# Performance work log

Measured on AMD Instinct MI355X. Metric: run time of the kernel, lower is better.

Reference implementation:

```python
import jax, jax.numpy as jnp
import numpy as np

B, S, H, F, E, K = 4, 2048, 1024, 3584, 8, 2
CAP_FACTOR = 1.25


def setup_inputs() -> dict:
    key = jax.random.key(0)
    k1, k2, k3, k4, k5 = jax.random.split(key, 5)
    s_h = 1.0 / np.sqrt(H)
    s_f = 1.0 / np.sqrt(F)
    return {
        "hidden_states": jax.random.normal(k1, (B, S, H), dtype=jnp.float32),
        "gate_w": jax.random.normal(k2, (E, H), dtype=jnp.float32) * s_h,
        "w1": jax.random.normal(k3, (E, H, F), dtype=jnp.float32) * s_h,
        "w2": jax.random.normal(k4, (E, F, H), dtype=jnp.float32) * s_f,
        "w3": jax.random.normal(k5, (E, H, F), dtype=jnp.float32) * s_h,
    }


def _moe_forward(hidden_states, gate_w, w1, w2, w3):
    b, s, h = hidden_states.shape
    dtype = hidden_states.dtype
    x = hidden_states.reshape(-1, h)  # [B*S, H]
    router_logits = x @ gate_w.T  # [B*S, E]
    expert_weights = jax.nn.softmax(router_logits.astype(jnp.float32), axis=1)
    _, selected_experts = jax.lax.top_k(expert_weights, K)  # [B*S, K]

    top_k_idx = selected_experts.reshape(b, s, K)
    probs = expert_weights.reshape(b, s, E)

    capacity = int(s * K / E * CAP_FACTOR)  # expert capacity per batch

    # dispatch/combine masks (Mixtral 'dropping' implementation)
    expert_mask = jax.nn.one_hot(top_k_idx, E, dtype=jnp.int32)  # [b,s,K,E]
    mask_fused = expert_mask.reshape(b, s * K, E)
    count_fused = jnp.cumsum(mask_fused, axis=1)  # running count per expert
    count = count_fused.reshape(b, s, K, E)
    trunc_mask = expert_mask * (count <= capacity).astype(jnp.int32)
    combined_mask = trunc_mask.sum(axis=2)  # [b,s,E]
    masked_probs = probs * combined_mask  # drop over-capacity tokens

    pos_fused = mask_fused * count_fused
    pos = pos_fused.reshape(b, s, K, E)
    combined_pos = pos.sum(axis=2) * combined_mask  # [b,s,E], 1-based slot
    pos_in_cap = jax.nn.one_hot(combined_pos, capacity + 1, dtype=jnp.int32)
    combine_mask = masked_probs[..., None] * pos_in_cap  # [b,s,E,cap+1]
    combine_mask = combine_mask[..., 1:].astype(dtype)  # drop slot 0 (dropped tokens)
    dispatch_mask = (combine_mask != 0).astype(dtype)  # [b,s,E,cap]

    # dispatch tokens into per-expert capacity buffers
    dispatch = jnp.einsum('bsm,bsec->ebcm', hidden_states, dispatch_mask)
    # expert FFN (SwiGLU)
    h1 = jnp.einsum('ebcm,emh->ebch', dispatch, w1)
    h3 = jnp.einsum('ebcm,emh->ebch', dispatch, w3)
    expert_out = jnp.einsum('ebch,ehm->ebcm', jax.nn.silu(h1) * h3, w2)
    # combine back to token order with routing probabilities
    final = jnp.einsum('ebcm,bsec->bsm', expert_out, combine_mask)
    return final


def reference(hidden_states, gate_w, w1, w2, w3):
    return _moe_forward(hidden_states, gate_w, w1, w2, w3)
```

## Files before the change

### kernel.cpp

```cpp
#include <hip/hip_runtime.h>
#include <hip/hip_bf16.h>
#include <math.h>

#define B_   4
#define S_   2048
#define H_   1024
#define F_   3584
#define E_   8
#define TOPK 2
#define CAP  640
#define M_   (B_*CAP)
#define NTOK (B_*S_)

typedef __attribute__((ext_vector_type(8))) short short8;
typedef __attribute__((ext_vector_type(4))) float f32x4;
typedef __attribute__((ext_vector_type(4))) unsigned short us4;

static __device__ __forceinline__ unsigned short f2bf(float f) {
  __hip_bfloat16 h = __float2bfloat16(f);
  return *reinterpret_cast<unsigned short*>(&h);
}
static __device__ __forceinline__ float bf2f(unsigned short u) {
  unsigned int x = ((unsigned int)u) << 16;
  float f;
  __builtin_memcpy(&f, &x, 4);
  return f;
}

static __device__ __forceinline__ void gload16(const void* g, void* l) {
  __builtin_amdgcn_global_load_lds((const __attribute__((address_space(1))) void*)g,
                                   (__attribute__((address_space(3))) void*)l, 16, 0, 0);
}

#define BAR() __builtin_amdgcn_s_barrier()
#define WLG() asm volatile("s_waitcnt lgkmcnt(0)" ::: "memory")
#define WVM4() asm volatile("s_waitcnt vmcnt(4)" ::: "memory")

__global__ __launch_bounds__(64) void k_router(const float* __restrict__ hs,
                                               const float* __restrict__ gw,
                                               int* __restrict__ e01,
                                               float* __restrict__ p01) {
  int t = blockIdx.x;
  int lane = threadIdx.x;
  const float4* xv = (const float4*)(hs + (size_t)t * H_);
  float4 xr[4];
#pragma unroll
  for (int i = 0; i < 4; ++i) xr[i] = xv[lane + i * 64];
  float logit[E_];
#pragma unroll
  for (int e = 0; e < E_; ++e) {
    const float4* gv = (const float4*)(gw + (size_t)e * H_);
    float acc = 0.f;
#pragma unroll
    for (int i = 0; i < 4; ++i) {
      float4 g = gv[lane + i * 64];
      acc += xr[i].x * g.x + xr[i].y * g.y + xr[i].z * g.z + xr[i].w * g.w;
    }
#pragma unroll
    for (int off = 32; off > 0; off >>= 1) acc += __shfl_xor(acc, off);
    logit[e] = acc;
  }
  float mx = logit[0];
#pragma unroll
  for (int e = 1; e < E_; ++e) mx = fmaxf(mx, logit[e]);
  float p[E_], s = 0.f;
#pragma unroll
  for (int e = 0; e < E_; ++e) { p[e] = expf(logit[e] - mx); s += p[e]; }
  float inv = 1.f / s;
  int e0 = 0;
#pragma unroll
  for (int e = 1; e < E_; ++e) if (p[e] > p[e0]) e0 = e;
  int e1 = (e0 == 0) ? 1 : 0;
#pragma unroll
  for (int e = 0; e < E_; ++e) if (e != e0 && p[e] > p[e1]) e1 = e;
  if (lane == 0) {
    e01[t * 2 + 0] = e0;
    e01[t * 2 + 1] = e1;
    p01[t * 2 + 0] = p[e0] * inv;
    p01[t * 2 + 1] = p[e1] * inv;
  }
}

__global__ __launch_bounds__(256) void k_positions(const int* __restrict__ e01,
                                                   int* __restrict__ pos,
                                                   int* __restrict__ disp) {
  int b = blockIdx.x, tid = threadIdx.x;
  __shared__ unsigned char eid[S_ * TOPK];
  __shared__ int part[256];
  for (int i = tid; i < E_ * CAP; i += 256)
    disp[((size_t)(i / CAP) * B_ + b) * CAP + (i % CAP)] = -1;
  for (int i = tid; i < S_ * TOPK; i += 256)
    eid[i] = (unsigned char)e01[b * S_ * TOPK + i];
  __syncthreads();
  const int per = (S_ * TOPK) / 256;
  int base = tid * per;
  for (int e = 0; e < E_; ++e) {
    int cnt = 0;
    for (int j = 0; j < per; ++j) cnt += (eid[base + j] == e) ? 1 : 0;
    part[tid] = cnt;
    __syncthreads();
    for (int off = 1; off < 256; off <<= 1) {
      int v = part[tid];
      int add = (tid >= off) ? part[tid - off] : 0;
      __syncthreads();
      part[tid] = v + add;
      __syncthreads();
    }
    int run = part[tid] - cnt;
    for (int j = 0; j < per; ++j) {
      int sl = base + j;
      if (eid[sl] == e) {
        ++run;
        int p = (run <= CAP) ? (run - 1) : -1;
        pos[b * S_ * TOPK + sl] = p;
        if (p >= 0) disp[((size_t)e * B_ + b) * CAP + p] = sl >> 1;
      }
    }
    __syncthreads();
  }
}

__global__ __launch_bounds__(256) void k_transpose(const float* __restrict__ in,
                                                   unsigned short* __restrict__ outp,
                                                   int R, int C, int ileave, int half,
                                                   size_t ostride_e) {
  __shared__ unsigned short ls[64][72];
  int e = blockIdx.z, tc = blockIdx.x, tr = blockIdx.y, tid = threadIdx.x;
  const float* src = in + (size_t)e * R * C + (size_t)tr * 64 * C + (size_t)tc * 64;
#pragma unroll
  for (int i = 0; i < 16; ++i) {
    int row = i * 4 + (tid >> 6), col = tid & 63;
    ls[row][col] = f2bf(src[(size_t)row * C + col]);
  }
  __syncthreads();
  unsigned short* dbase = outp + (size_t)e * ostride_e;
#pragma unroll
  for (int i = 0; i < 4; ++i) {
    int orow = i * 16 + (tid >> 4), oc = (tid & 15) * 4;
    int gr = tc * 64 + orow;
    int ri = ileave ? ((gr & ~15) * 2 + (gr & 15) + half * 16) : gr;
    us4 v = {ls[oc + 0][orow], ls[oc + 1][orow], ls[oc + 2][orow], ls[oc + 3][orow]};
    *(us4*)&dbase[(size_t)ri * R + tr * 64 + oc] = v;
  }
}

__global__ __launch_bounds__(256) void k_dispatch(const float* __restrict__ hs,
                                                  const int* __restrict__ disp,
                                                  unsigned short* __restrict__ xd) {
  int slot = blockIdx.x;
  int tid = threadIdx.x;
  int tok = disp[slot];
  int b = (slot / CAP) % B_;
  us4 v;
  if (tok >= 0) {
    const float4* src = (const float4*)(hs + ((size_t)b * S_ + tok) * H_);
    float4 f = src[tid];
    v = {f2bf(f.x), f2bf(f.y), f2bf(f.z), f2bf(f.w)};
  } else {
    v = {0, 0, 0, 0};
  }
  *(us4*)&xd[(size_t)slot * H_ + tid * 4] = v;
}

#define STAGE(src, opsel, dreg, t, h) do {                                   \
    int _ro = ((dreg)*4 + (opsel) + (h)) * 8192 + tid * 8;                   \
    const unsigned short* _p = (src) + (size_t)(t) * 64 + (h) * 32;          \
    gload16(_p, &lds[_ro]);                                                  \
    gload16(_p + (size_t)128 * KTOT, &lds[_ro + 4096]);                      \
  } while (0)

#define RD_A(d, h) {                                                         \
    const unsigned short* _pa = &lds[((d)*4 + (h)) * 8192 + aoff];           \
    _Pragma("unroll") for (int m = 0; m < 8; ++m)                            \
      a[m] = *(const short8*)&_pa[m * 512];                                  \
  }
#define RD_B(d, h, nh) {                                                     \
    const unsigned short* _pb = &lds[((d)*4 + 2 + (h)) * 8192 + boff];       \
    b0 = *(const short8*)&_pb[(nh) * 1024];                                  \
    b1 = *(const short8*)&_pb[(nh) * 1024 + 512];                            \
  }
#define MFMA8(nh) {                                                          \
    __builtin_amdgcn_s_setprio(1);                                           \
    _Pragma("unroll") for (int m = 0; m < 8; ++m) {                          \
      acc[m][(nh)*2]   = __builtin_amdgcn_mfma_f32_16x16x32_bf16(a[m], b0, acc[m][(nh)*2],   0, 0, 0); \
      acc[m][(nh)*2+1] = __builtin_amdgcn_mfma_f32_16x16x32_bf16(a[m], b1, acc[m][(nh)*2+1], 0, 0, 0); \
    }                                                                        \
    __builtin_amdgcn_s_setprio(0);                                           \
  }

template <int KTOT, bool SWIGLU, int MT, int NTN, int NTOTB>
__global__ __launch_bounds__(512, 2) void k_gemm256(const unsigned short* __restrict__ Aall,
                                                    const unsigned short* __restrict__ Ball,
                                                    unsigned short* __restrict__ Cout) {
  constexpr int NT = KTOT / 64;
  constexpr int NI = NT / 2;
  __shared__ __align__(16) unsigned short lds[65536];

  const int nwg = MT * NTN * E_;
  int lid = blockIdx.x;
  int sw = (lid & 7) * (nwg >> 3) + (lid >> 3);
  int e = sw / (MT * NTN);
  int rem = sw - e * (MT * NTN);
  int tn = rem / MT, tm = rem - tn * MT;

  int tid = threadIdx.x, li = tid & 63, wid = tid >> 6;
  int wm = wid >> 2, wn = wid & 3;

  int rS = tid >> 2;
  int gS = (tid & 3) ^ ((tid >> 3) & 3);
  const unsigned short* srcA = Aall + ((size_t)e * M_ + (size_t)tm * 256 + rS) * KTOT + gS * 8;
  const unsigned short* srcB = Ball + ((size_t)e * NTOTB + (size_t)tn * 256 + rS) * KTOT + gS * 8;

  int sA = (li >> 4) ^ ((li >> 1) & 3);
  int aoff = (wm * 128 + (li & 15)) * 32 + sA * 8;
  int boff = (wn * 64 + (li & 15)) * 32 + sA * 8;

  f32x4 acc[8][4] = {};
  short8 a[8], b0, b1;

  STAGE(srcA, 0, 0, 0, 0);
  STAGE(srcB, 2, 0, 0, 0);
  STAGE(srcA, 0, 0, 0, 1);
  STAGE(srcB, 2, 0, 0, 1);
  STAGE(srcA, 0, 1, 1, 0);
  STAGE(srcB, 2, 1, 1, 0);
  WVM4();
  BAR();

#pragma unroll 1
  for (int i = 0; i < NI; ++i) {
    int t1 = 2 * i + 1;
    int t2 = (2 * i + 2 < NT) ? 2 * i + 2 : NT - 1;
    int t3 = (2 * i + 3 < NT) ? 2 * i + 3 : NT - 1;
    RD_A(0, 0); RD_B(0, 0, 0); STAGE(srcA, 0, 1, t1, 1);
    BAR(); WLG(); MFMA8(0); BAR();
    RD_B(0, 0, 1); STAGE(srcB, 2, 1, t1, 1);
    BAR(); WLG(); MFMA8(1); BAR();
    RD_A(0, 1); RD_B(0, 1, 0); STAGE(srcA, 0, 0, t2, 0);
    BAR(); WLG(); MFMA8(0); BAR();
    RD_B(0, 1, 1); STAGE(srcB, 2, 0, t2, 0); WVM4();
    BAR(); WLG(); MFMA8(1); BAR();
    RD_A(1, 0); RD_B(1, 0, 0); STAGE(srcA, 0, 0, t2, 1);
    BAR(); WLG(); MFMA8(0); BAR();
    RD_B(1, 0, 1); STAGE(srcB, 2, 0, t2, 1);
    BAR(); WLG(); MFMA8(1); BAR();
    RD_A(1, 1); RD_B(1, 1, 0); STAGE(srcA, 0, 1, t3, 0);
    BAR(); WLG(); MFMA8(0); BAR();
    RD_B(1, 1, 1); STAGE(srcB, 2, 1, t3, 0); WVM4();
    BAR(); WLG(); MFMA8(1); BAR();
  }

  int r0 = tm * 256 + wm * 128 + ((li >> 4) << 2);
  if constexpr (SWIGLU) {
    unsigned short* out = Cout + (size_t)e * M_ * F_;
#pragma unroll
    for (int m = 0; m < 8; ++m)
#pragma unroll
      for (int u = 0; u < 2; ++u) {
        int col = (tn * 8 + wn * 2 + u) * 16 + (li & 15);
#pragma unroll
        for (int j = 0; j < 4; ++j) {
          float h1 = acc[m][2 * u][j], h3 = acc[m][2 * u + 1][j];
          float sg = 1.f / (1.f + __expf(-h1));
          out[(size_t)(r0 + m * 16 + j) * F_ + col] = f2bf(h1 * sg * h3);
        }
      }
  } else {
    unsigned short* out = Cout + (size_t)e * M_ * NTOTB;
#pragma unroll
    for (int m = 0; m < 8; ++m)
#pragma unroll
      for (int n = 0; n < 4; ++n) {
        int col = tn * 256 + wn * 64 + n * 16 + (li & 15);
#pragma unroll
        for (int j = 0; j < 4; ++j)
          out[(size_t)(r0 + m * 16 + j) * NTOTB + col] = f2bf(acc[m][n][j]);
      }
  }
}

__global__ __launch_bounds__(256) void k_combine(const unsigned short* __restrict__ Oe,
                                                 const int* __restrict__ e01,
                                                 const float* __restrict__ p01,
                                                 const int* __restrict__ pos,
                                                 float* __restrict__ outp) {
  int t = blockIdx.x;
  int b = t / S_;
  int tid = threadIdx.x;
  float4 acc = {0.f, 0.f, 0.f, 0.f};
#pragma unroll
  for (int k = 0; k < TOPK; ++k) {
    int p = pos[t * 2 + k];
    if (p >= 0) {
      int e = e01[t * 2 + k];
      float w = p01[t * 2 + k];
      size_t row = (size_t)e * M_ + (size_t)b * CAP + p;
      us4 v = *(const us4*)&Oe[row * H_ + tid * 4];
      acc.x += w * bf2f(v[0]);
      acc.y += w * bf2f(v[1]);
      acc.z += w * bf2f(v[2]);
      acc.w += w * bf2f(v[3]);
    }
  }
  *(float4*)&outp[(size_t)t * H_ + tid * 4] = acc;
}

extern "C" void kernel_launch(void* const* d_in, const int* in_sizes, int n_in,
                              void* d_out, int out_size, void* d_ws, size_t ws_size,
                              hipStream_t stream) {
  const float* hs = (const float*)d_in[0];
  const float* gw = (const float*)d_in[1];
  const float* w1 = (const float*)d_in[2];
  const float* w2 = (const float*)d_in[3];
  const float* w3 = (const float*)d_in[4];

  char* ws = (char*)d_ws;
  size_t off = 0;
  auto take = [&](size_t bytes) -> char* {
    char* p = ws + off;
    off += (bytes + 255) & ~(size_t)255;
    return p;
  };
  int*            e01  = (int*)take((size_t)NTOK * 2 * 4);
  float*          p01  = (float*)take((size_t)NTOK * 2 * 4);
  int*            pos  = (int*)take((size_t)NTOK * 2 * 4);
  int*            disp = (int*)take((size_t)E_ * B_ * CAP * 4);
  unsigned short* w13t = (unsigned short*)take((size_t)E_ * 2 * F_ * H_ * 2);
  unsigned short* w2t  = (unsigned short*)take((size_t)E_ * H_ * F_ * 2);
  unsigned short* xd   = (unsigned short*)take((size_t)E_ * M_ * H_ * 2);
  unsigned short* act  = (unsigned short*)take((size_t)E_ * M_ * F_ * 2);
  unsigned short* oe   = (unsigned short*)take((size_t)E_ * M_ * H_ * 2);

  k_router<<<NTOK, 64, 0, stream>>>(hs, gw, e01, p01);
  k_positions<<<B_, 256, 0, stream>>>(e01, pos, disp);
  k_transpose<<<dim3(F_ / 64, H_ / 64, E_), 256, 0, stream>>>(w1, w13t, H_, F_, 1, 0, (size_t)2 * F_ * H_);
  k_transpose<<<dim3(F_ / 64, H_ / 64, E_), 256, 0, stream>>>(w3, w13t, H_, F_, 1, 1, (size_t)2 * F_ * H_);
  k_transpose<<<dim3(H_ / 64, F_ / 64, E_), 256, 0, stream>>>(w2, w2t, F_, H_, 0, 0, (size_t)H_ * F_);
  k_dispatch<<<E_ * B_ * CAP, 256, 0, stream>>>(hs, disp, xd);
  k_gemm256<H_, true, M_ / 256, (2 * F_) / 256, 2 * F_><<<(M_ / 256) * ((2 * F_) / 256) * E_, 512, 0, stream>>>(xd, w13t, act);
  k_gemm256<F_, false, M_ / 256, H_ / 256, H_><<<(M_ / 256) * (H_ / 256) * E_, 512, 0, stream>>>(act, w2t, oe);
  k_combine<<<NTOK, 256, 0, stream>>>(oe, e01, p01, pos, (float*)d_out);
}
```

Baseline: 634.0 us.

## Parametrize GEMM N-tile width and simplify pipeline to four phases per iteration

The GEMM kernel gains an NREG template parameter so the N tile can be 256 (first GEMM) or 128 (second GEMM), shrinking LDS use and doubling the number of workgroups for the down-projection, which had only 320 tiles. The inner loop is restructured from eight half-phases into four phases that each load all B fragments and issue every MFMA at once, with adjusted vmcnt and lgkmcnt waits. This raises parallelism for the down GEMM at the cost of less operand reuse per tile. It also changes barrier and wait placement in the first GEMM.

```diff
diff --git a/kernel.cpp b/kernel.cpp
--- a/kernel.cpp
+++ b/kernel.cpp
@@ -34,7 +34,6 @@
 
 #define BAR() __builtin_amdgcn_s_barrier()
 #define WLG() asm volatile("s_waitcnt lgkmcnt(0)" ::: "memory")
-#define WVM4() asm volatile("s_waitcnt vmcnt(4)" ::: "memory")
 
 __global__ __launch_bounds__(64) void k_router(const float* __restrict__ hs,
                                                const float* __restrict__ gw,
@@ -162,39 +161,58 @@
   *(us4*)&xd[(size_t)slot * H_ + tid * 4] = v;
 }
 
-#define STAGE(src, opsel, dreg, t, h) do {                                   \
-    int _ro = ((dreg)*4 + (opsel) + (h)) * 8192 + tid * 8;                   \
-    const unsigned short* _p = (src) + (size_t)(t) * 64 + (h) * 32;          \
-    gload16(_p, &lds[_ro]);                                                  \
-    gload16(_p + (size_t)128 * KTOT, &lds[_ro + 4096]);                      \
-  } while (0)
-
-#define RD_A(d, h) {                                                         \
-    const unsigned short* _pa = &lds[((d)*4 + (h)) * 8192 + aoff];           \
-    _Pragma("unroll") for (int m = 0; m < 8; ++m)                            \
-      a[m] = *(const short8*)&_pa[m * 512];                                  \
-  }
-#define RD_B(d, h, nh) {                                                     \
-    const unsigned short* _pb = &lds[((d)*4 + 2 + (h)) * 8192 + boff];       \
-    b0 = *(const short8*)&_pb[(nh) * 1024];                                  \
-    b1 = *(const short8*)&_pb[(nh) * 1024 + 512];                            \
-  }
-#define MFMA8(nh) {                                                          \
-    __builtin_amdgcn_s_setprio(1);                                           \
-    _Pragma("unroll") for (int m = 0; m < 8; ++m) {                          \
-      acc[m][(nh)*2]   = __builtin_amdgcn_mfma_f32_16x16x32_bf16(a[m], b0, acc[m][(nh)*2],   0, 0, 0); \
-      acc[m][(nh)*2+1] = __builtin_amdgcn_mfma_f32_16x16x32_bf16(a[m], b1, acc[m][(nh)*2+1], 0, 0, 0); \
-    }                                                                        \
-    __builtin_amdgcn_s_setprio(0);                                           \
-  }
-
-template <int KTOT, bool SWIGLU, int MT, int NTN, int NTOTB>
+#define STAGE_A(d, h, t) {                                                    \
+    int _ro = ((d) * 2 + (h)) * 8192 + tid * 8;                               \
+    const unsigned short* _p = srcA + (size_t)(t) * 64 + (h) * 32;            \
+    gload16(_p, &lds[_ro]);                                                   \
+    gload16(_p + (size_t)128 * KTOT, &lds[_ro + 4096]);                       \
+  }
+#define STAGE_B(d, h, t) {                                                    \
+    int _ro = 32768 + ((d) * 2 + (h)) * BREG + tid * 8;                       \
+    const unsigned short* _p = srcB + (size_t)(t) * 64 + (h) * 32;            \
+    gload16(_p, &lds[_ro]);                                                   \
+    if (NREG == 4) gload16(_p + (size_t)128 * KTOT, &lds[_ro + 4096]);        \
+  }
+#define RD_A(d, h) {                                                          \
+    const unsigned short* _pa = &lds[((d) * 2 + (h)) * 8192 + aoff];          \
+    _Pragma("unroll") for (int m = 0; m < 8; ++m)                             \
+      a[m] = *(const short8*)&_pa[m * 512];                                   \
+  }
+#define RD_B(d, h) {                                                          \
+    const unsigned short* _pb = &lds[32768 + ((d) * 2 + (h)) * BREG + boff];  \
+    _Pragma("unroll") for (int n = 0; n < NREG; ++n)                          \
+      bfr[n] = *(const short8*)&_pb[n * 512];                                 \
+  }
+#define MFMA_ALL() {                                                          \
+    __builtin_amdgcn_s_setprio(1);                                            \
+    _Pragma("unroll") for (int m = 0; m < 8; ++m)                             \
+      _Pragma("unroll") for (int n = 0; n < NREG; ++n)                        \
+        acc[m][n] = __builtin_amdgcn_mfma_f32_16x16x32_bf16(a[m], bfr[n], acc[m][n], 0, 0, 0); \
+    __builtin_amdgcn_s_setprio(0);                                            \
+  }
+#define WVM() {                                                               \
+    if (NREG == 4) asm volatile("s_waitcnt vmcnt(8)" ::: "memory");           \
+    else           asm volatile("s_waitcnt vmcnt(6)" ::: "memory");           \
+  }
+#define PHASE(pd, ph, sd, sh, st) {                                           \
+    RD_A(pd, ph); RD_B(pd, ph);                                               \
+    STAGE_A(sd, sh, st); STAGE_B(sd, sh, st);                                 \
+    asm volatile("s_waitcnt lgkmcnt(8)" ::: "memory");                        \
+    BAR(); WLG();                                                             \
+    MFMA_ALL();                                                               \
+    WVM(); BAR();                                                             \
+  }
+
+template <int KTOT, bool SWIGLU, int NREG, int MT, int NTN, int NTOTB>
 __global__ __launch_bounds__(512, 2) void k_gemm256(const unsigned short* __restrict__ Aall,
                                                     const unsigned short* __restrict__ Ball,
                                                     unsigned short* __restrict__ Cout) {
   constexpr int NT = KTOT / 64;
   constexpr int NI = NT / 2;
-  __shared__ __align__(16) unsigned short lds[65536];
+  constexpr int BREG = 2048 * NREG;
+  constexpr int LDS_US = 32768 + 4 * BREG;
+  constexpr int BN = NREG * 64;
+  __shared__ __align__(16) unsigned short lds[LDS_US];
 
   const int nwg = MT * NTN * E_;
   int lid = blockIdx.x;
@@ -209,22 +227,19 @@
   int rS = tid >> 2;
   int gS = (tid & 3) ^ ((tid >> 3) & 3);
   const unsigned short* srcA = Aall + ((size_t)e * M_ + (size_t)tm * 256 + rS) * KTOT + gS * 8;
-  const unsigned short* srcB = Ball + ((size_t)e * NTOTB + (size_t)tn * 256 + rS) * KTOT + gS * 8;
+  const unsigned short* srcB = Ball + ((size_t)e * NTOTB + (size_t)tn * BN + rS) * KTOT + gS * 8;
 
   int sA = (li >> 4) ^ ((li >> 1) & 3);
   int aoff = (wm * 128 + (li & 15)) * 32 + sA * 8;
-  int boff = (wn * 64 + (li & 15)) * 32 + sA * 8;
-
-  f32x4 acc[8][4] = {};
-  short8 a[8], b0, b1;
-
-  STAGE(srcA, 0, 0, 0, 0);
-  STAGE(srcB, 2, 0, 0, 0);
-  STAGE(srcA, 0, 0, 0, 1);
-  STAGE(srcB, 2, 0, 0, 1);
-  STAGE(srcA, 0, 1, 1, 0);
-  STAGE(srcB, 2, 1, 1, 0);
-  WVM4();
+  int boff = (wn * (16 * NREG) + (li & 15)) * 32 + sA * 8;
+
+  f32x4 acc[8][NREG] = {};
+  short8 a[8], bfr[NREG];
+
+  STAGE_A(0, 0, 0); STAGE_B(0, 0, 0);
+  STAGE_A(0, 1, 0); STAGE_B(0, 1, 0);
+  STAGE_A(1, 0, 1); STAGE_B(1, 0, 1);
+  WVM();
   BAR();
 
 #pragma unroll 1
@@ -232,22 +247,10 @@
     int t1 = 2 * i + 1;
     int t2 = (2 * i + 2 < NT) ? 2 * i + 2 : NT - 1;
     int t3 = (2 * i + 3 < NT) ? 2 * i + 3 : NT - 1;
-    RD_A(0, 0); RD_B(0, 0, 0); STAGE(srcA, 0, 1, t1, 1);
-    BAR(); WLG(); MFMA8(0); BAR();
-    RD_B(0, 0, 1); STAGE(srcB, 2, 1, t1, 1);
-    BAR(); WLG(); MFMA8(1); BAR();
-    RD_A(0, 1); RD_B(0, 1, 0); STAGE(srcA, 0, 0, t2, 0);
-    BAR(); WLG(); MFMA8(0); BAR();
-    RD_B(0, 1, 1); STAGE(srcB, 2, 0, t2, 0); WVM4();
-    BAR(); WLG(); MFMA8(1); BAR();
-    RD_A(1, 0); RD_B(1, 0, 0); STAGE(srcA, 0, 0, t2, 1);
-    BAR(); WLG(); MFMA8(0); BAR();
-    RD_B(1, 0, 1); STAGE(srcB, 2, 0, t2, 1);
-    BAR(); WLG(); MFMA8(1); BAR();
-    RD_A(1, 1); RD_B(1, 1, 0); STAGE(srcA, 0, 1, t3, 0);
-    BAR(); WLG(); MFMA8(0); BAR();
-    RD_B(1, 1, 1); STAGE(srcB, 2, 1, t3, 0); WVM4();
-    BAR(); WLG(); MFMA8(1); BAR();
+    PHASE(0, 0, 1, 1, t1);
+    PHASE(0, 1, 0, 0, t2);
+    PHASE(1, 0, 0, 1, t2);
+    PHASE(1, 1, 1, 0, t3);
   }
 
   int r0 = tm * 256 + wm * 128 + ((li >> 4) << 2);
@@ -270,8 +273,8 @@
 #pragma unroll
     for (int m = 0; m < 8; ++m)
 #pragma unroll
-      for (int n = 0; n < 4; ++n) {
-        int col = tn * 256 + wn * 64 + n * 16 + (li & 15);
+      for (int n = 0; n < NREG; ++n) {
+        int col = tn * BN + wn * (16 * NREG) + n * 16 + (li & 15);
 #pragma unroll
         for (int j = 0; j < 4; ++j)
           out[(size_t)(r0 + m * 16 + j) * NTOTB + col] = f2bf(acc[m][n][j]);
@@ -337,7 +340,9 @@
   k_transpose<<<dim3(F_ / 64, H_ / 64, E_), 256, 0, stream>>>(w3, w13t, H_, F_, 1, 1, (size_t)2 * F_ * H_);
   k_transpose<<<dim3(H_ / 64, F_ / 64, E_), 256, 0, stream>>>(w2, w2t, F_, H_, 0, 0, (size_t)H_ * F_);
   k_dispatch<<<E_ * B_ * CAP, 256, 0, stream>>>(hs, disp, xd);
-  k_gemm256<H_, true, M_ / 256, (2 * F_) / 256, 2 * F_><<<(M_ / 256) * ((2 * F_) / 256) * E_, 512, 0, stream>>>(xd, w13t, act);
-  k_gemm256<F_, false, M_ / 256, H_ / 256, H_><<<(M_ / 256) * (H_ / 256) * E_, 512, 0, stream>>>(act, w2t, oe);
+  k_gemm256<H_, true, 4, M_ / 256, (2 * F_) / 256, 2 * F_>
+      <<<(M_ / 256) * ((2 * F_) / 256) * E_, 512, 0, stream>>>(xd, w13t, act);
+  k_gemm256<F_, false, 2, M_ / 256, H_ / 128, H_>
+      <<<(M_ / 256) * (H_ / 128) * E_, 512, 0, stream>>>(act, w2t, oe);
   k_combine<<<NTOK, 256, 0, stream>>>(oe, e01, p01, pos, (float*)d_out);
 }
```

Measured after the change: 672.7 us. +6.1%, slower.
